# Performance work log

Measured on AMD Instinct MI355X. Metric: run time of the kernel, lower is better.

The kernel has to match this reference:

```python
import jax, jax.numpy as jnp
import numpy as np

B, N, NIN = 32, 128, 64
MSG_HID, MSG_OUT, N_HID, N_OUT = 256, 64, 256, 64
E = N * (N - 1)  # fully connected, no self loops


def setup_inputs() -> dict:
    key = jax.random.key(0)
    ks = jax.random.split(key, 12)

    # one-hot incidence matrices (NRI convention)
    off = np.ones((N, N), dtype=np.float32) - np.eye(N, dtype=np.float32)
    recv_idx, send_idx = np.where(off)
    eye = np.eye(N, dtype=np.float32)
    rel_rec = jnp.asarray(eye[recv_idx])    # [E, N]
    rel_send = jnp.asarray(eye[send_idx])   # [E, N]

    s = 0.05
    inp = {
        "inputs": jax.random.normal(ks[0], (B, N, NIN), jnp.float32),
        "rel_rec": rel_rec,
        "rel_send": rel_send,
        "rel_types": jax.random.uniform(ks[1], (B, E, 2), jnp.float32),
        "msg_fc1_w": jax.random.normal(ks[2], (MSG_HID, 2 * NIN), jnp.float32) * s,
        "msg_fc1_b": jnp.zeros((MSG_HID,), jnp.float32),
        "msg_fc2_w": jax.random.normal(ks[3], (MSG_OUT, MSG_HID), jnp.float32) * s,
        "msg_fc2_b": jnp.zeros((MSG_OUT,), jnp.float32),
        "out_fc1_w": jax.random.normal(ks[4], (N_HID, MSG_OUT), jnp.float32) * s,
        "out_fc1_b": jnp.zeros((N_HID,), jnp.float32),
        "out_fc2_w": jax.random.normal(ks[5], (N_HID, N_HID), jnp.float32) * s,
        "out_fc2_b": jnp.zeros((N_HID,), jnp.float32),
        "out_fc3_w": jax.random.normal(ks[6], (N_OUT, N_HID), jnp.float32) * s,
        "out_fc3_b": jnp.zeros((N_OUT,), jnp.float32),
    }
    return inp


def reference(inputs, rel_rec, rel_send, rel_types,
              msg_fc1_w, msg_fc1_b, msg_fc2_w, msg_fc2_b,
              out_fc1_w, out_fc1_b, out_fc2_w, out_fc2_b,
              out_fc3_w, out_fc3_b):
    # node2edge: gather sender / receiver node features via one-hot matmul
    senders = jnp.einsum('en,bnf->bef', rel_send, inputs)    # [B,E,NIN]
    receivers = jnp.einsum('en,bnf->bef', rel_rec, inputs)   # [B,E,NIN]
    pre_msg = jnp.concatenate([senders, receivers], axis=-1)  # [B,E,2*NIN]

    all_msgs = jnp.zeros(pre_msg.shape[:2] + (MSG_OUT,), pre_msg.dtype)
    for i in range(2):  # edge-type loop (shared weights, as in the original)
        msg = jax.nn.relu(pre_msg @ msg_fc1_w.T + msg_fc1_b)
        msg = jax.nn.relu(msg @ msg_fc2_w.T + msg_fc2_b)
        all_msgs = all_msgs + msg * rel_types[:, :, i:i + 1]

    # edge2node: scatter-add messages to receiving nodes
    agg_msgs = jnp.einsum('bem,en->bnm', all_msgs, rel_rec)   # [B,N,MSG_OUT]

    pred = jax.nn.relu(agg_msgs @ out_fc1_w.T + out_fc1_b)
    pred = jax.nn.relu(pred @ out_fc2_w.T + out_fc2_b)
    pred = pred @ out_fc3_w.T + out_fc3_b                      # [B,N,N_OUT]
    return pred
```

## Files before the change

### kernel.cpp

```cpp
#include <hip/hip_runtime.h>

#define BB 32
#define NN_ 128
#define NIN 64
#define MH 256
#define MO 64
#define NH 256
#define NO 64
#define EDGES 16256

typedef _Float16 half8 __attribute__((ext_vector_type(8)));
typedef __attribute__((ext_vector_type(4))) float f32x4;


static __device__ __forceinline__ unsigned short f2h(float f) {
    return __builtin_bit_cast(unsigned short, (_Float16)f);
}

static __device__ __forceinline__ half8 pack8h(float4 f0, float4 f1) {
    uint4 u;
    u.x = __builtin_bit_cast(unsigned, __builtin_amdgcn_cvt_pkrtz(f0.x, f0.y));
    u.y = __builtin_bit_cast(unsigned, __builtin_amdgcn_cvt_pkrtz(f0.z, f0.w));
    u.z = __builtin_bit_cast(unsigned, __builtin_amdgcn_cvt_pkrtz(f1.x, f1.y));
    u.w = __builtin_bit_cast(unsigned, __builtin_amdgcn_cvt_pkrtz(f1.z, f1.w));
    return __builtin_bit_cast(half8, u);
}

static __device__ __forceinline__ half8 addrelu(uint4 s, uint4 p) {
    half8 a = __builtin_bit_cast(half8, s) + __builtin_bit_cast(half8, p);
    half8 z = {};
    return __builtin_elementwise_max(a, z);
}

__global__ __launch_bounds__(256) void prep_kernel(
    const float* __restrict__ x, const float* __restrict__ W1,
    const float* __restrict__ b1, const float* __restrict__ W2,
    const float* __restrict__ O1, const float* __restrict__ O2,
    const float* __restrict__ O3,
    unsigned short* __restrict__ psb, unsigned short* __restrict__ prb,
    unsigned short* __restrict__ w2b, unsigned short* __restrict__ o1b,
    unsigned short* __restrict__ o2b, unsigned short* __restrict__ o3b)
{
    int blk = blockIdx.x;
    int t = threadIdx.x;
    if (blk < 256) {
        int row0 = blk << 4;
        int b = blk >> 3;
        int w = t >> 6, lane = t & 63, ml = lane & 15, q = lane >> 4;

        half8 aX[2];
        #pragma unroll
        for (int s = 0; s < 2; ++s) {
            const float* base = x + (size_t)(row0 + ml) * NIN + s * 32 + q * 8;
            aX[s] = pack8h(*(const float4*)base, *(const float4*)(base + 4));
        }

        #pragma unroll
        for (int half = 0; half < 2; ++half) {
            #pragma unroll
            for (int nt = 0; nt < 4; ++nt) {
                int col = w * 64 + nt * 16 + ml;
                const float* wrow = W1 + (size_t)col * (2 * NIN) + half * 64 + q * 8;
                f32x4 acc = (f32x4){0.f, 0.f, 0.f, 0.f};
                #pragma unroll
                for (int s = 0; s < 2; ++s) {
                    half8 bw = pack8h(*(const float4*)(wrow + 32 * s),
                                      *(const float4*)(wrow + 32 * s + 4));
                    acc = __builtin_amdgcn_mfma_f32_16x16x32_f16(aX[s], bw, acc, 0, 0, 0);
                }
                if (half == 0) {
                    #pragma unroll
                    for (int reg = 0; reg < 4; ++reg) {
                        int n = (row0 + q * 4 + reg) & 127;
                        psb[((size_t)(b * 32 + (col >> 3)) * NN_ + n) * 8 + (col & 7)]
                            = f2h(acc[reg]);
                    }
                } else {
                    float bv = b1[col];
                    #pragma unroll
                    for (int reg = 0; reg < 4; ++reg) {
                        int n = (row0 + q * 4 + reg) & 127;
                        prb[((size_t)(b * NN_) + n) * MH + col] = f2h(acc[reg] + bv);
                    }
                }
            }
        }
    } else if (blk < 320) {
        int i = ((blk - 256) << 8) + t;
        int kc4 = i >> 9, rem = i & 511;
        int n = rem >> 3, k7 = i & 7;
        w2b[i] = f2h(W2[n * MH + kc4 * 8 + k7]);
    } else {
        int i = ((blk - 320) << 8) + t;
        if (i < 16384)       o1b[i]         = f2h(O1[i]);
        else if (i < 81920)  o2b[i - 16384] = f2h(O2[i - 16384]);
        else                 o3b[i - 81920] = f2h(O3[i - 81920]);
    }
}

__global__ __launch_bounds__(512) void edge_node_kernel(
    const float* __restrict__ rt, const float* __restrict__ b2,
    const unsigned short* __restrict__ psb, const unsigned short* __restrict__ prb,
    const unsigned short* __restrict__ w2b,
    const unsigned short* __restrict__ o1b, const float* __restrict__ b1o,
    const unsigned short* __restrict__ o2b, const float* __restrict__ b2o,
    const unsigned short* __restrict__ o3b, const float* __restrict__ b3o,
    float* __restrict__ out)
{
    int blk = blockIdx.x;
    int t = threadIdx.x;
    int wv = t >> 6;
    int lane = t & 63;
    int ml = lane & 15, q = lane >> 4;

    int b = blk >> 4;
    int rbase = (blk & 15) << 3;

    __shared__ float rtw_lds[2][128];
    __shared__ float red[2][8][64];
    __shared__ float aggL[16][68];
    __shared__ unsigned short h1L[16][264];
    __shared__ unsigned short h2L[16][264];

    aggL[8 + wv][lane] = 0.f;

    float b2c[4];
    #pragma unroll
    for (int nt = 0; nt < 4; ++nt) b2c[nt] = b2[16 * nt + ml];

    const uint4* ps4 = (const uint4*)psb + (size_t)b * (32 * NN_);
    const uint4* w24 = (const uint4*)w2b;

    int slot = 16 * wv + ml;

    #pragma unroll 1
    for (int un = 0; un < 4; ++un) {
        int r0 = rbase + un * 2;

        __syncthreads();
        if (t < 256) {
            int rr = t >> 7, s = t & 127;
            int r = r0 + rr;
            float v = 0.f;
            if (s != r) {
                int e = r * 127 + s - (s > r ? 1 : 0);
                const float* p = rt + ((size_t)(b * EDGES + e)) * 2;
                v = p[0] + p[1];
            }
            rtw_lds[rr][s] = v;
        }
        __syncthreads();

        const uint4* pr4_0 = (const uint4*)(prb + ((size_t)(b * NN_ + r0)) * MH);
        const uint4* pr4_1 = (const uint4*)(prb + ((size_t)(b * NN_ + r0 + 1)) * MH);

        f32x4 acc[2][4];
        #pragma unroll
        for (int rr = 0; rr < 2; ++rr)
            #pragma unroll
            for (int nt = 0; nt < 4; ++nt)
                acc[rr][nt] = (f32x4){0.f, 0.f, 0.f, 0.f};

        #pragma unroll
        for (int kc = 0; kc < 8; ++kc) {
            int kc4 = 4 * kc + q;
            uint4 us  = ps4[kc4 * NN_ + slot];
            uint4 up0 = pr4_0[kc4];
            uint4 up1 = pr4_1[kc4];

            half8 a0 = addrelu(us, up0);
            half8 a1 = addrelu(us, up1);

            #pragma unroll
            for (int nt = 0; nt < 4; ++nt) {
                half8 bw = __builtin_bit_cast(half8, w24[kc4 * 64 + 16 * nt + ml]);
                acc[0][nt] = __builtin_amdgcn_mfma_f32_16x16x32_f16(a0, bw, acc[0][nt], 0, 0, 0);
                acc[1][nt] = __builtin_amdgcn_mfma_f32_16x16x32_f16(a1, bw, acc[1][nt], 0, 0, 0);
            }
        }

        #pragma unroll
        for (int rr = 0; rr < 2; ++rr) {
            float colsum[4] = {0.f, 0.f, 0.f, 0.f};
            int srow = 16 * wv + 4 * q;
            #pragma unroll
            for (int reg = 0; reg < 4; ++reg) {
                float rw = rtw_lds[rr][srow + reg];
                #pragma unroll
                for (int nt = 0; nt < 4; ++nt)
                    colsum[nt] += fmaxf(acc[rr][nt][reg] + b2c[nt], 0.f) * rw;
            }
            #pragma unroll
            for (int nt = 0; nt < 4; ++nt) {
                colsum[nt] += __shfl_xor(colsum[nt], 16);
                colsum[nt] += __shfl_xor(colsum[nt], 32);
            }
            if (lane < 16) {
                #pragma unroll
                for (int nt = 0; nt < 4; ++nt)
                    red[rr][wv][16 * nt + ml] = colsum[nt];
            }
        }
        __syncthreads();
        if (t < 128) {
            int rr = t >> 6, o = t & 63;
            float s = 0.f;
            #pragma unroll
            for (int w8 = 0; w8 < 8; ++w8) s += red[rr][w8][o];
            aggL[un * 2 + rr][o] = s;
        }
    }
    __syncthreads();

    half8 aA[2];
    #pragma unroll
    for (int s = 0; s < 2; ++s) {
        const float* base = &aggL[ml][32 * s + q * 8];
        aA[s] = pack8h(*(const float4*)base, *(const float4*)(base + 4));
    }

    #pragma unroll
    for (int nt = 0; nt < 2; ++nt) {
        int ntg = wv * 2 + nt;
        f32x4 acc = (f32x4){0.f, 0.f, 0.f, 0.f};
        #pragma unroll
        for (int s = 0; s < 2; ++s) {
            half8 bw = *(const half8*)(o1b + (size_t)(ntg * 16 + ml) * 64 + 32 * s + q * 8);
            acc = __builtin_amdgcn_mfma_f32_16x16x32_f16(aA[s], bw, acc, 0, 0, 0);
        }
        float bv = b1o[ntg * 16 + ml];
        #pragma unroll
        for (int reg = 0; reg < 4; ++reg)
            h1L[q * 4 + reg][ntg * 16 + ml] = f2h(fmaxf(acc[reg] + bv, 0.f));
    }
    __syncthreads();

    half8 aH[8];
    #pragma unroll
    for (int ks = 0; ks < 8; ++ks)
        aH[ks] = *(const half8*)&h1L[ml][32 * ks + q * 8];
    #pragma unroll
    for (int nt = 0; nt < 2; ++nt) {
        int ntg = wv * 2 + nt;
        const unsigned short* wrow = o2b + (size_t)(ntg * 16 + ml) * NH + q * 8;
        f32x4 acc = (f32x4){0.f, 0.f, 0.f, 0.f};
        #pragma unroll
        for (int ks = 0; ks < 8; ++ks) {
            half8 bw = *(const half8*)(wrow + 32 * ks);
            acc = __builtin_amdgcn_mfma_f32_16x16x32_f16(aH[ks], bw, acc, 0, 0, 0);
        }
        float bv = b2o[ntg * 16 + ml];
        #pragma unroll
        for (int reg = 0; reg < 4; ++reg)
            h2L[q * 4 + reg][ntg * 16 + ml] = f2h(fmaxf(acc[reg] + bv, 0.f));
    }
    __syncthreads();

    if (wv < 4) {
        #pragma unroll
        for (int ks = 0; ks < 8; ++ks)
            aH[ks] = *(const half8*)&h2L[ml][32 * ks + q * 8];
        const unsigned short* wrow = o3b + (size_t)(wv * 16 + ml) * NH + q * 8;
        f32x4 acc = (f32x4){0.f, 0.f, 0.f, 0.f};
        #pragma unroll
        for (int ks = 0; ks < 8; ++ks) {
            half8 bw = *(const half8*)(wrow + 32 * ks);
            acc = __builtin_amdgcn_mfma_f32_16x16x32_f16(aH[ks], bw, acc, 0, 0, 0);
        }
        float bv = b3o[wv * 16 + ml];
        if (q < 2) {
            #pragma unroll
            for (int reg = 0; reg < 4; ++reg)
                out[(size_t)(b * NN_ + rbase + q * 4 + reg) * NO + wv * 16 + ml]
                    = acc[reg] + bv;
        }
    }
}

extern "C" void kernel_launch(void* const* d_in, const int* in_sizes, int n_in,
                              void* d_out, int out_size, void* d_ws, size_t ws_size,
                              hipStream_t stream) {
    const float* x   = (const float*)d_in[0];
    const float* rt  = (const float*)d_in[3];
    const float* W1  = (const float*)d_in[4];
    const float* b1  = (const float*)d_in[5];
    const float* W2  = (const float*)d_in[6];
    const float* b2  = (const float*)d_in[7];
    const float* O1  = (const float*)d_in[8];
    const float* b1o = (const float*)d_in[9];
    const float* O2  = (const float*)d_in[10];
    const float* b2o = (const float*)d_in[11];
    const float* O3  = (const float*)d_in[12];
    const float* b3o = (const float*)d_in[13];

    float* ws  = (float*)d_ws;
    unsigned short* psb = (unsigned short*)ws;
    unsigned short* prb = (unsigned short*)(ws + 524288);
    unsigned short* w2b = (unsigned short*)(ws + 1048576);
    unsigned short* o1b = (unsigned short*)(ws + 1056768);
    unsigned short* o2b = (unsigned short*)(ws + 1064960);
    unsigned short* o3b = (unsigned short*)(ws + 1097728);
    float* out = (float*)d_out;

    hipLaunchKernelGGL(prep_kernel, dim3(704), dim3(256), 0, stream,
                       x, W1, b1, W2, O1, O2, O3, psb, prb, w2b, o1b, o2b, o3b);
    hipLaunchKernelGGL(edge_node_kernel, dim3(512), dim3(512), 0, stream,
                       rt, b2, psb, prb, w2b, o1b, b1o, o2b, b2o, o3b, b3o, out);
}
```

Baseline: 136.5 us.

## Stage W2 in LDS, hoist sender loads and rel-type weights out of loop

```diff
diff --git a/kernel.cpp b/kernel.cpp
--- a/kernel.cpp
+++ b/kernel.cpp
@@ -116,41 +116,53 @@
     int b = blk >> 4;
     int rbase = (blk & 15) << 3;
 
-    __shared__ float rtw_lds[2][128];
+    __shared__ uint4 w2L[2048];
+    __shared__ float rtwA[4][2][128];
     __shared__ float red[2][8][64];
     __shared__ float aggL[16][68];
     __shared__ unsigned short h1L[16][264];
     __shared__ unsigned short h2L[16][264];
 
+    {
+        const uint4* w24 = (const uint4*)w2b;
+        #pragma unroll
+        for (int i = 0; i < 4; ++i)
+            w2L[t + 512 * i] = w24[t + 512 * i];
+    }
+    #pragma unroll
+    for (int j = 0; j < 2; ++j) {
+        int idx = 2 * t + j;
+        int un = idx >> 8, rr = (idx >> 7) & 1, s = idx & 127;
+        int r = rbase + un * 2 + rr;
+        float v = 0.f;
+        if (s != r) {
+            int e = r * 127 + s - (s > r ? 1 : 0);
+            const float* p = rt + ((size_t)(b * EDGES + e)) * 2;
+            v = p[0] + p[1];
+        }
+        rtwA[un][rr][s] = v;
+    }
+
     aggL[8 + wv][lane] = 0.f;
 
     float b2c[4];
     #pragma unroll
     for (int nt = 0; nt < 4; ++nt) b2c[nt] = b2[16 * nt + ml];
 
-    const uint4* ps4 = (const uint4*)psb + (size_t)b * (32 * NN_);
-    const uint4* w24 = (const uint4*)w2b;
-
     int slot = 16 * wv + ml;
+    uint4 usr[8];
+    {
+        const uint4* ps4 = (const uint4*)psb + (size_t)b * (32 * NN_);
+        #pragma unroll
+        for (int kc = 0; kc < 8; ++kc)
+            usr[kc] = ps4[(4 * kc + q) * NN_ + slot];
+    }
+
+    __syncthreads();
 
     #pragma unroll 1
     for (int un = 0; un < 4; ++un) {
         int r0 = rbase + un * 2;
-
-        __syncthreads();
-        if (t < 256) {
-            int rr = t >> 7, s = t & 127;
-            int r = r0 + rr;
-            float v = 0.f;
-            if (s != r) {
-                int e = r * 127 + s - (s > r ? 1 : 0);
-                const float* p = rt + ((size_t)(b * EDGES + e)) * 2;
-                v = p[0] + p[1];
-            }
-            rtw_lds[rr][s] = v;
-        }
-        __syncthreads();
-
         const uint4* pr4_0 = (const uint4*)(prb + ((size_t)(b * NN_ + r0)) * MH);
         const uint4* pr4_1 = (const uint4*)(prb + ((size_t)(b * NN_ + r0 + 1)) * MH);
 
@@ -164,16 +176,15 @@
         #pragma unroll
         for (int kc = 0; kc < 8; ++kc) {
             int kc4 = 4 * kc + q;
-            uint4 us  = ps4[kc4 * NN_ + slot];
             uint4 up0 = pr4_0[kc4];
             uint4 up1 = pr4_1[kc4];
 
-            half8 a0 = addrelu(us, up0);
-            half8 a1 = addrelu(us, up1);
+            half8 a0 = addrelu(usr[kc], up0);
+            half8 a1 = addrelu(usr[kc], up1);
 
             #pragma unroll
             for (int nt = 0; nt < 4; ++nt) {
-                half8 bw = __builtin_bit_cast(half8, w24[kc4 * 64 + 16 * nt + ml]);
+                half8 bw = __builtin_bit_cast(half8, w2L[kc4 * 64 + 16 * nt + ml]);
                 acc[0][nt] = __builtin_amdgcn_mfma_f32_16x16x32_f16(a0, bw, acc[0][nt], 0, 0, 0);
                 acc[1][nt] = __builtin_amdgcn_mfma_f32_16x16x32_f16(a1, bw, acc[1][nt], 0, 0, 0);
             }
@@ -185,7 +196,7 @@
             int srow = 16 * wv + 4 * q;
             #pragma unroll
             for (int reg = 0; reg < 4; ++reg) {
-                float rw = rtw_lds[rr][srow + reg];
+                float rw = rtwA[un][rr][srow + reg];
                 #pragma unroll
                 for (int nt = 0; nt < 4; ++nt)
                     colsum[nt] += fmaxf(acc[rr][nt][reg] + b2c[nt], 0.f) * rw;
@@ -209,8 +220,8 @@
             for (int w8 = 0; w8 < 8; ++w8) s += red[rr][w8][o];
             aggL[un * 2 + rr][o] = s;
         }
-    }
-    __syncthreads();
+        __syncthreads();
+    }
 
     half8 aA[2];
     #pragma unroll
```

Measured after the change: 125.7 us. 1.09x faster.
